# Kernel tuning notes

Hardware: AMD Instinct MI355X
Metric: run time of the kernel (lower is better)

Reference implementation:

```python
import jax, jax.numpy as jnp
import numpy as np

NUM_CLASSES = 3
LAMBDA_COORD = 5.0
B, A, N = 1048576, 3, 8  # batch, anchors (hardcoded 3 in source), gt boxes per image


def setup_inputs() -> dict:
    key = jax.random.key(0)
    k1, k2, k3 = jax.random.split(key, 3)
    predictions = jax.random.normal(k1, (B, A, 5 + NUM_CLASSES), dtype=jnp.float32)
    gt_boxes = jax.random.uniform(k2, (B, N, 4), dtype=jnp.float32)  # x,y,w,h
    gt_classes = jax.random.randint(k3, (B, N), 0, NUM_CLASSES, dtype=jnp.int32)
    return {"predictions": predictions, "gt_boxes": gt_boxes, "gt_classes": gt_classes}


def reference(predictions, gt_boxes, gt_classes):
    batch = predictions.shape[0]
    # decode predictions, shapes (B, A)
    px = jax.nn.sigmoid(predictions[..., 0])
    py = jax.nn.sigmoid(predictions[..., 1])
    pw = predictions[..., 2]
    ph = predictions[..., 3]
    pconf = jax.nn.sigmoid(predictions[..., 4])
    plogits = predictions[..., 5:]  # (B, A, C)

    # pred corners (B, A, 1)
    px1 = (px - pw / 2)[..., None]; px2 = (px + pw / 2)[..., None]
    py1 = (py - ph / 2)[..., None]; py2 = (py + ph / 2)[..., None]
    # gt corners (B, 1, N)
    gx = gt_boxes[..., 0][:, None, :]; gy = gt_boxes[..., 1][:, None, :]
    gw = gt_boxes[..., 2][:, None, :]; gh = gt_boxes[..., 3][:, None, :]
    gx1 = gx - gw / 2; gx2 = gx + gw / 2
    gy1 = gy - gh / 2; gy2 = gy + gh / 2

    inter_w = jnp.clip(jnp.minimum(px2, gx2) - jnp.maximum(px1, gx1), 0.0)
    inter_h = jnp.clip(jnp.minimum(py2, gy2) - jnp.maximum(py1, gy1), 0.0)
    inter = inter_w * inter_h                              # (B, A, N)
    pred_area = (px2 - px1) * (py2 - py1)                  # (B, A, 1)
    gt_area = (gx2 - gx1) * (gy2 - gy1)                    # (B, 1, N)
    iou = inter / (pred_area + gt_area - inter + 1e-6)     # (B, A, N)

    best_iou = jnp.max(iou, axis=-1)                       # (B, A)
    best_idx = jnp.argmax(iou, axis=-1)                    # (B, A) -- first max, matches strict-> loop
    matched = best_iou > 0.5                               # (B, A)

    mb = jnp.take_along_axis(gt_boxes, best_idx[:, :, None], axis=1)   # (B, A, 4)
    mcls = jnp.take_along_axis(gt_classes, best_idx, axis=1)           # (B, A)

    # coordinate loss: per-scalar mse on matched anchors
    coord = (px - mb[..., 0]) ** 2 + (py - mb[..., 1]) ** 2 \
          + (pw - mb[..., 2]) ** 2 + (ph - mb[..., 3]) ** 2
    coord_loss = jnp.sum(jnp.where(matched, coord, 0.0))

    # confidence BCE, target 1 if matched else 0 (torch BCE clamps log at -100)
    logp = jnp.maximum(jnp.log(pconf), -100.0)
    log1mp = jnp.maximum(jnp.log1p(-pconf), -100.0)
    conf_loss = jnp.sum(jnp.where(matched, -logp, -log1mp))

    # class cross-entropy on matched anchors
    logsm = jax.nn.log_softmax(plogits, axis=-1)                        # (B, A, C)
    nll = -jnp.take_along_axis(logsm, mcls[..., None], axis=-1)[..., 0]  # (B, A)
    class_loss = jnp.sum(jnp.where(matched, nll, 0.0))

    total = LAMBDA_COORD * coord_loss + conf_loss + class_loss
    return total / batch
```

## Files before the change

kernel.cpp:

```cpp
#include <hip/hip_runtime.h>

#define B_SIZE 1048576
#define NBLK   4096

__device__ __forceinline__ float frcp(float x) { return __builtin_amdgcn_rcpf(x); }

__global__ __launch_bounds__(256) void yolo_loss_kernel(
    const float* __restrict__ pred,
    const float* __restrict__ gt_boxes,
    const int*   __restrict__ gt_classes,
    double* __restrict__ part) {
    __shared__ float sP[4][64 * 25];
    __shared__ float sG[4][64 * 33];
    __shared__ float sRed[4];

    const int tid  = threadIdx.x;
    const int wave = tid >> 6;
    const int lane = tid & 63;
    const int wb   = blockIdx.x * 256 + wave * 64;

    const float4* pA = reinterpret_cast<const float4*>(pred     + (size_t)wb * 24);
    const float4* gA = reinterpret_cast<const float4*>(gt_boxes + (size_t)wb * 32);
    float4 vp[6], vg[8];
    #pragma unroll
    for (int k = 0; k < 6; ++k) vp[k] = pA[k * 64 + lane];
    #pragma unroll
    for (int k = 0; k < 8; ++k) vg[k] = gA[k * 64 + lane];
    const int4* cme = reinterpret_cast<const int4*>(gt_classes + (size_t)(wb + lane) * 8);
    const int4 c0 = cme[0], c1 = cme[1];

    float* sp = sP[wave];
    float* sg = sG[wave];
    #pragma unroll
    for (int k = 0; k < 6; ++k) {
        const unsigned f = k * 64 + lane;
        const unsigned bl = f / 6u, of = f % 6u;
        float* d = &sp[bl * 25 + of * 4];
        d[0] = vp[k].x; d[1] = vp[k].y; d[2] = vp[k].z; d[3] = vp[k].w;
    }
    #pragma unroll
    for (int k = 0; k < 8; ++k) {
        const unsigned f = k * 64 + lane;
        const unsigned bl = f >> 3, of = f & 7;
        float* d = &sg[bl * 33 + of * 4];
        d[0] = vg[k].x; d[1] = vg[k].y; d[2] = vg[k].z; d[3] = vg[k].w;
    }
    float pr[24];
    #pragma unroll
    for (int w = 0; w < 24; ++w) pr[w] = sp[lane * 25 + w];
    float gb[32];
    #pragma unroll
    for (int w = 0; w < 32; ++w) gb[w] = sg[lane * 33 + w];
    const int gc[8] = {c0.x, c0.y, c0.z, c0.w, c1.x, c1.y, c1.z, c1.w};

    float total = 0.0f;
    #pragma unroll
    for (int a = 0; a < 3; ++a) {
        const float* p = pr + a * 8;
        const float px = frcp(1.0f + __expf(-p[0]));
        const float py = frcp(1.0f + __expf(-p[1]));
        const float pw = p[2];
        const float ph = p[3];
        const float z  = p[4];
        const float px1 = px - pw * 0.5f, px2 = px + pw * 0.5f;
        const float py1 = py - ph * 0.5f, py2 = py + ph * 0.5f;
        const float pa_eps = (px2 - px1) * (py2 - py1) + 1e-6f;

        float best_iou = -3.4e38f;
        int best_idx = 0;
        #pragma unroll
        for (int n = 0; n < 8; ++n) {
            const float gx = gb[n*4+0], gy = gb[n*4+1];
            const float gw = gb[n*4+2], gh = gb[n*4+3];
            const float hw = gw * 0.5f, hh = gh * 0.5f;
            const float iw = fmaxf(fminf(px2, gx + hw) - fmaxf(px1, gx - hw), 0.0f);
            const float ih = fmaxf(fminf(py2, gy + hh) - fmaxf(py1, gy - hh), 0.0f);
            const float inter = iw * ih;
            const float iou = inter * frcp((pa_eps + gw * gh) - inter);
            const bool upd = iou > best_iou;
            best_iou = upd ? iou : best_iou;
            best_idx = upd ? n : best_idx;
        }
        const bool matched = best_iou > 0.5f;

        float mbx = gb[0], mby = gb[1], mbw = gb[2], mbh = gb[3];
        int mcls = gc[0];
        #pragma unroll
        for (int n = 1; n < 8; ++n) {
            const bool s = (best_idx == n);
            mbx = s ? gb[n*4+0] : mbx;
            mby = s ? gb[n*4+1] : mby;
            mbw = s ? gb[n*4+2] : mbw;
            mbh = s ? gb[n*4+3] : mbh;
            mcls = s ? gc[n] : mcls;
        }

        const float az = fabsf(z);
        const float c  = __logf(1.0f + __expf(-az));
        const float sp_pos = fmaxf(z, 0.0f) + c;
        const float sp_neg = fmaxf(-z, 0.0f) + c;
        total += fminf(matched ? sp_neg : sp_pos, 100.0f);

        if (matched) {
            const float dx = px - mbx, dy = py - mby;
            const float dw = pw - mbw, dh = ph - mbh;
            total += 5.0f * (dx*dx + dy*dy + dw*dw + dh*dh);
            const float l0 = p[5], l1 = p[6], l2 = p[7];
            const float m = fmaxf(l0, fmaxf(l1, l2));
            const float lse = m + __logf(__expf(l0-m) + __expf(l1-m) + __expf(l2-m));
            const float sel = (mcls == 0) ? l0 : ((mcls == 1) ? l1 : l2);
            total += lse - sel;
        }
    }

    #pragma unroll
    for (int off = 32; off > 0; off >>= 1)
        total += __shfl_down(total, off, 64);
    if (lane == 0) sRed[wave] = total;
    __syncthreads();
    if (tid == 0) {
        part[blockIdx.x] = (double)sRed[0] + (double)sRed[1]
                         + (double)sRed[2] + (double)sRed[3];
    }
}

__global__ __launch_bounds__(256) void yolo_reduce_kernel(
    const double* __restrict__ part, float* __restrict__ out) {
    double s = 0.0;
    #pragma unroll
    for (int k = 0; k < NBLK / 256; ++k)
        s += part[threadIdx.x + k * 256];
    #pragma unroll
    for (int off = 32; off > 0; off >>= 1)
        s += __shfl_down(s, off, 64);
    __shared__ double r[4];
    const int lane = threadIdx.x & 63;
    const int wave = threadIdx.x >> 6;
    if (lane == 0) r[wave] = s;
    __syncthreads();
    if (threadIdx.x == 0)
        out[0] = (float)((r[0] + r[1] + r[2] + r[3]) / (double)B_SIZE);
}

extern "C" void kernel_launch(void* const* d_in, const int* in_sizes, int n_in,
                              void* d_out, int out_size, void* d_ws, size_t ws_size,
                              hipStream_t stream) {
    const float* pred       = (const float*)d_in[0];
    const float* gt_boxes   = (const float*)d_in[1];
    const int*   gt_classes = (const int*)d_in[2];
    float* out   = (float*)d_out;
    double* part = (double*)d_ws;

    yolo_loss_kernel<<<NBLK, 256, 0, stream>>>(pred, gt_boxes, gt_classes, part);
    yolo_reduce_kernel<<<1, 256, 0, stream>>>(part, out);
}
```

Baseline: 275.4 us.

## Reuse one XOR-swizzled float4 LDS buffer, drop block barrier, write per-wave partials

Replaces the two padded scalar LDS staging arrays with a single per-wave float4 buffer using an XOR swizzle, reused first for predictions and then for gt boxes. This cuts LDS footprint and turns scalar LDS reads and writes into 128-bit accesses. The block-level __syncthreads reduction is removed: each wave writes its own double partial, and the final reduce kernel sums four times as many partials. A launch-bounds occupancy hint of 5 is also added, which may constrain register allocation.

New measurement: 284.9 us. +3.5%, slower.

```diff
diff --git a/kernel.cpp b/kernel.cpp
--- a/kernel.cpp
+++ b/kernel.cpp
@@ -2,17 +2,16 @@
 
 #define B_SIZE 1048576
 #define NBLK   4096
+#define NPART  (NBLK * 4)
 
 __device__ __forceinline__ float frcp(float x) { return __builtin_amdgcn_rcpf(x); }
 
-__global__ __launch_bounds__(256) void yolo_loss_kernel(
+__global__ __launch_bounds__(256, 5) void yolo_loss_kernel(
     const float* __restrict__ pred,
     const float* __restrict__ gt_boxes,
     const int*   __restrict__ gt_classes,
     double* __restrict__ part) {
-    __shared__ float sP[4][64 * 25];
-    __shared__ float sG[4][64 * 33];
-    __shared__ float sRed[4];
+    __shared__ float4 sBuf[4][64][8];
 
     const int tid  = threadIdx.x;
     const int wave = tid >> 6;
@@ -29,28 +28,33 @@
     const int4* cme = reinterpret_cast<const int4*>(gt_classes + (size_t)(wb + lane) * 8);
     const int4 c0 = cme[0], c1 = cme[1];
 
-    float* sp = sP[wave];
-    float* sg = sG[wave];
+    float4 (*buf)[8] = sBuf[wave];
+
     #pragma unroll
     for (int k = 0; k < 6; ++k) {
-        const unsigned f = k * 64 + lane;
+        const unsigned f  = k * 64 + lane;
         const unsigned bl = f / 6u, of = f % 6u;
-        float* d = &sp[bl * 25 + of * 4];
-        d[0] = vp[k].x; d[1] = vp[k].y; d[2] = vp[k].z; d[3] = vp[k].w;
-    }
-    #pragma unroll
-    for (int k = 0; k < 8; ++k) {
-        const unsigned f = k * 64 + lane;
-        const unsigned bl = f >> 3, of = f & 7;
-        float* d = &sg[bl * 33 + of * 4];
-        d[0] = vg[k].x; d[1] = vg[k].y; d[2] = vg[k].z; d[3] = vg[k].w;
+        buf[bl][of ^ (bl & 7u)] = vp[k];
     }
     float pr[24];
     #pragma unroll
-    for (int w = 0; w < 24; ++w) pr[w] = sp[lane * 25 + w];
+    for (int s = 0; s < 6; ++s) {
+        const float4 t = buf[lane][s ^ (lane & 7)];
+        pr[s*4+0] = t.x; pr[s*4+1] = t.y; pr[s*4+2] = t.z; pr[s*4+3] = t.w;
+    }
+
+    #pragma unroll
+    for (int k = 0; k < 8; ++k) {
+        const unsigned f  = k * 64 + lane;
+        const unsigned bl = f >> 3, of = f & 7;
+        buf[bl][of ^ (bl & 7u)] = vg[k];
+    }
     float gb[32];
     #pragma unroll
-    for (int w = 0; w < 32; ++w) gb[w] = sg[lane * 33 + w];
+    for (int s = 0; s < 8; ++s) {
+        const float4 t = buf[lane][s ^ (lane & 7)];
+        gb[s*4+0] = t.x; gb[s*4+1] = t.y; gb[s*4+2] = t.z; gb[s*4+3] = t.w;
+    }
     const int gc[8] = {c0.x, c0.y, c0.z, c0.w, c1.x, c1.y, c1.z, c1.w};
 
     float total = 0.0f;
@@ -116,19 +120,15 @@
     #pragma unroll
     for (int off = 32; off > 0; off >>= 1)
         total += __shfl_down(total, off, 64);
-    if (lane == 0) sRed[wave] = total;
-    __syncthreads();
-    if (tid == 0) {
-        part[blockIdx.x] = (double)sRed[0] + (double)sRed[1]
-                         + (double)sRed[2] + (double)sRed[3];
-    }
+    if (lane == 0)
+        part[(size_t)blockIdx.x * 4 + wave] = (double)total;
 }
 
 __global__ __launch_bounds__(256) void yolo_reduce_kernel(
     const double* __restrict__ part, float* __restrict__ out) {
     double s = 0.0;
     #pragma unroll
-    for (int k = 0; k < NBLK / 256; ++k)
+    for (int k = 0; k < NPART / 256; ++k)
         s += part[threadIdx.x + k * 256];
     #pragma unroll
     for (int off = 32; off > 0; off >>= 1)
```
